# Kernel tuning notes

Hardware: AMD Instinct MI355X
Metric: run time of the kernel (lower is better)

Reference implementation:

```python
import jax, jax.numpy as jnp
import numpy as np

NUM_HEADS = 16


def setup_inputs() -> dict:
    key = jax.random.key(0)
    ks = jax.random.split(key, 8)
    B, S, D = 2, 2048, 1024
    q = jax.random.normal(ks[0], (B, S, D), dtype=jnp.float32)
    k = jax.random.normal(ks[1], (B, S, D), dtype=jnp.float32)
    v = jax.random.normal(ks[2], (B, S, D), dtype=jnp.float32)
    mask = jax.random.randint(ks[3], (1, 1, S, S), 0, 2, dtype=jnp.int32)
    sc = 1.0 / np.sqrt(D)
    wq = jax.random.normal(ks[4], (D, D), dtype=jnp.float32) * sc
    wk = jax.random.normal(ks[5], (D, D), dtype=jnp.float32) * sc
    wv = jax.random.normal(ks[6], (D, D), dtype=jnp.float32) * sc
    wout = jax.random.normal(ks[7], (D, D), dtype=jnp.float32) * sc
    return {"q": q, "k": k, "v": v, "mask": mask,
            "wq": wq, "wk": wk, "wv": wv, "wout": wout}


def reference(q, k, v, mask, wq, wk, wv, wout):
    B, S, D = q.shape
    H = NUM_HEADS
    hd = D // H

    def proj(x, w):
        # nn.Linear(bias=False): x @ w.T, then split heads -> [B,H,S,hd]
        return (x @ w.T).reshape(B, -1, H, hd).transpose(0, 2, 1, 3)

    qh, kh, vh = proj(q, wq), proj(k, wk), proj(v, wv)
    scale = jnp.asarray(hd, q.dtype) ** 0.5
    scores = jnp.einsum('bhqd,bhkd->bhqk', qh, kh) / scale  # [B,H,S,S]
    att = jax.nn.softmax(scores, axis=-1)
    # NOTE: original applies masked_fill AFTER softmax with value -1e-9
    att = jnp.where(mask == 0, jnp.asarray(-1e-9, att.dtype), att)
    out = jnp.einsum('bhqk,bhkd->bhqd', att, vh)  # [B,H,S,hd]
    out = out.transpose(0, 2, 1, 3).reshape(B, S, D)
    return out @ wout.T
```

## Files before the change

### kernel.cpp

```cpp
#include <hip/hip_runtime.h>
#include <stdint.h>


#define BATCH  2
#define S_LEN  2048
#define DMODEL 1024
#define NH     16
#define HD     64

typedef __bf16 bf16_t;
typedef short  short8 __attribute__((ext_vector_type(8)));
typedef float  f32x4  __attribute__((ext_vector_type(4)));

#define AS1 __attribute__((address_space(1)))
#define AS3 __attribute__((address_space(3)))

static constexpr size_t MB = (size_t)1 << 20;
static constexpr size_t WS_REQUIRED = 112 * MB;
#define OFF_XHI(z)  ((size_t)(z) * 16 * MB)
#define OFF_XLO(z)  (OFF_XHI(z) + 8 * MB)
#define OFF_WHI(z)  (48 * MB + (size_t)(z) * 4 * MB)
#define OFF_WLO(z)  (OFF_WHI(z) + 2 * MB)
#define OFF_PHI(z)  (64 * MB + (size_t)(z) * 16 * MB)
#define OFF_PLO(z)  (OFF_PHI(z) + 8 * MB)
#define OFF_OHI     ((size_t)0)
#define OFF_OLO     (8 * MB)
#define OFF_MASKB   (16 * MB)

__device__ __forceinline__ f32x4 mfma_bf16(short8 a, short8 b, f32x4 c) {
    return __builtin_amdgcn_mfma_f32_16x16x32_bf16(a, b, c, 0, 0, 0);
}

__device__ __forceinline__ short8 ld8(const bf16_t* p) {
    return *reinterpret_cast<const short8*>(p);
}

__global__ void cvt_split_kernel(const float* __restrict__ x,
                                 bf16_t* __restrict__ hi, bf16_t* __restrict__ lo,
                                 int n) {
    int i = (blockIdx.x * blockDim.x + threadIdx.x) * 4;
    if (i >= n) return;
    const float4 v = *reinterpret_cast<const float4*>(x + i);
    float s[4] = {v.x, v.y, v.z, v.w};
    ushort hbits[4], lbits[4];
#pragma unroll
    for (int j = 0; j < 4; j++) {
        bf16_t hh = (bf16_t)s[j];
        bf16_t ll = (bf16_t)(s[j] - (float)hh);
        hbits[j] = __builtin_bit_cast(ushort, hh);
        lbits[j] = __builtin_bit_cast(ushort, ll);
    }
    *reinterpret_cast<ushort4*>(hi + i) = ushort4{hbits[0], hbits[1], hbits[2], hbits[3]};
    *reinterpret_cast<ushort4*>(lo + i) = ushort4{lbits[0], lbits[1], lbits[2], lbits[3]};
}

__global__ void cvt_mask_kernel(const int* __restrict__ m, bf16_t* __restrict__ mb, int n) {
    int i = (blockIdx.x * blockDim.x + threadIdx.x) * 4;
    if (i >= n) return;
    const int4 v = *reinterpret_cast<const int4*>(m + i);
    int s[4] = {v.x, v.y, v.z, v.w};
    ushort b[4];
#pragma unroll
    for (int j = 0; j < 4; j++) {
        bf16_t t = (bf16_t)(s[j] ? 1.0f : 0.0f);
        b[j] = __builtin_bit_cast(ushort, t);
    }
    *reinterpret_cast<ushort4*>(mb + i) = ushort4{b[0], b[1], b[2], b[3]};
}

template <int FINAL>
__global__ __launch_bounds__(256, 2) void gemm_split_kernel(char* __restrict__ ws,
                                                            float* __restrict__ fout) {
    __shared__ __align__(16) bf16_t AsH[128 * 32];
    __shared__ __align__(16) bf16_t AsL[128 * 32];
    __shared__ __align__(16) bf16_t BsH[128 * 32];
    __shared__ __align__(16) bf16_t BsL[128 * 32];

    const int z = FINAL ? 3 : blockIdx.z;
    const bf16_t* Ahi = FINAL ? (const bf16_t*)(ws + OFF_OHI) : (const bf16_t*)(ws + OFF_XHI(z));
    const bf16_t* Alo = FINAL ? (const bf16_t*)(ws + OFF_OLO) : (const bf16_t*)(ws + OFF_XLO(z));
    const bf16_t* Bhi = (const bf16_t*)(ws + OFF_WHI(z));
    const bf16_t* Blo = (const bf16_t*)(ws + OFF_WLO(z));
    bf16_t* Ohi = FINAL ? nullptr : (bf16_t*)(ws + OFF_PHI(z));
    bf16_t* Olo = FINAL ? nullptr : (bf16_t*)(ws + OFF_PLO(z));
    const float scale = (!FINAL && z == 0) ? 0.125f : 1.0f;

    const int tid = threadIdx.x;
    const int lane = tid & 63, w = tid >> 6;
    const int wr = w >> 1, wc = w & 1;
    const int fr = lane & 15, fg = lane >> 4;
    const int m0 = blockIdx.x * 128, n0 = blockIdx.y * 128;
    const int K = 1024;

    f32x4 acc[4][4];
#pragma unroll
    for (int i = 0; i < 4; i++)
#pragma unroll
        for (int j = 0; j < 4; j++) acc[i][j] = f32x4{0.f, 0.f, 0.f, 0.f};

    AS3 bf16_t* asAH = (AS3 bf16_t*)AsH;
    AS3 bf16_t* asAL = (AS3 bf16_t*)AsL;
    AS3 bf16_t* asBH = (AS3 bf16_t*)BsH;
    AS3 bf16_t* asBL = (AS3 bf16_t*)BsL;

#pragma unroll 1
    for (int ks = 0; ks < K; ks += 32) {
        __syncthreads();
#pragma unroll
        for (int i = 0; i < 2; i++) {
            const int c = i * 256 + tid;
            const int row = c >> 2;
            const int ce = (c & 3) * 8;
            const size_t gA = (size_t)(m0 + row) * K + ks + ce;
            const size_t gB = (size_t)(n0 + row) * K + ks + ce;
            const size_t d = (size_t)(i * 256 + w * 64) * 8;
            __builtin_amdgcn_global_load_lds((const AS1 void*)(Ahi + gA), (AS3 void*)(asAH + d), 16, 0, 0);
            __builtin_amdgcn_global_load_lds((const AS1 void*)(Alo + gA), (AS3 void*)(asAL + d), 16, 0, 0);
            __builtin_amdgcn_global_load_lds((const AS1 void*)(Bhi + gB), (AS3 void*)(asBH + d), 16, 0, 0);
            __builtin_amdgcn_global_load_lds((const AS1 void*)(Blo + gB), (AS3 void*)(asBL + d), 16, 0, 0);
        }
        __syncthreads();

        short8 afh[4], afl[4], bfh[4], bfl[4];
#pragma unroll
        for (int i = 0; i < 4; i++) {
            const int ao = (wr * 64 + i * 16 + fr) * 32 + fg * 8;
            const int bo = (wc * 64 + i * 16 + fr) * 32 + fg * 8;
            afh[i] = ld8(&AsH[ao]);
            afl[i] = ld8(&AsL[ao]);
            bfh[i] = ld8(&BsH[bo]);
            bfl[i] = ld8(&BsL[bo]);
        }
#pragma unroll
        for (int i = 0; i < 4; i++)
#pragma unroll
            for (int j = 0; j < 4; j++) {
                acc[i][j] = mfma_bf16(afh[i], bfh[j], acc[i][j]);
                acc[i][j] = mfma_bf16(afh[i], bfl[j], acc[i][j]);
                acc[i][j] = mfma_bf16(afl[i], bfh[j], acc[i][j]);
            }
    }

#pragma unroll
    for (int i = 0; i < 4; i++) {
#pragma unroll
        for (int j = 0; j < 4; j++) {
            const int ncol = n0 + wc * 64 + j * 16 + fr;
#pragma unroll
            for (int r = 0; r < 4; r++) {
                const int m = m0 + wr * 64 + i * 16 + fg * 4 + r;
                const float val = acc[i][j][r] * scale;
                if (FINAL) {
                    fout[(size_t)m * DMODEL + ncol] = val;
                } else {
                    const bf16_t h = (bf16_t)val;
                    const bf16_t l = (bf16_t)(val - (float)h);
                    const int b = m >> 11, s = m & (S_LEN - 1);
                    const int hh = ncol >> 6, d = ncol & (HD - 1);
                    size_t idx;
                    if (z == 2) idx = ((size_t)(b * NH + hh) * HD + d) * S_LEN + s;
                    else        idx = ((size_t)(b * NH + hh) * S_LEN + s) * HD + d;
                    Ohi[idx] = h;
                    Olo[idx] = l;
                }
            }
        }
    }
}

__global__ __launch_bounds__(256, 2) void attn_kernel(char* __restrict__ ws) {
    __shared__ __align__(16) bf16_t KsH[2][8 * 64 * 8];
    __shared__ __align__(16) bf16_t KsL[2][8 * 64 * 8];
    __shared__ __align__(16) bf16_t VsH[2][8 * 64 * 8];
    __shared__ __align__(16) bf16_t VsL[2][8 * 64 * 8];

    const bf16_t* Qhi = (const bf16_t*)(ws + OFF_PHI(0));
    const bf16_t* Qlo = (const bf16_t*)(ws + OFF_PLO(0));
    const bf16_t* Khi = (const bf16_t*)(ws + OFF_PHI(1));
    const bf16_t* Klo = (const bf16_t*)(ws + OFF_PLO(1));
    const bf16_t* Vhi = (const bf16_t*)(ws + OFF_PHI(2));
    const bf16_t* Vlo = (const bf16_t*)(ws + OFF_PLO(2));
    const bf16_t* Mb  = (const bf16_t*)(ws + OFF_MASKB);
    bf16_t* Ohi = (bf16_t*)(ws + OFF_OHI);
    bf16_t* Olo = (bf16_t*)(ws + OFF_OLO);

    const int tid = threadIdx.x, lane = tid & 63, w = tid >> 6;
    const int fr = lane & 15, fg = lane >> 4;
    const int bh = blockIdx.y;
    const int q0 = blockIdx.x * 64;
    const int qrow = q0 + w * 16 + fr;
    const size_t qkBase = (size_t)bh * S_LEN * HD;
    const size_t vtBase = (size_t)bh * HD * S_LEN;

    size_t kSrc[2], vSrc[2];
#pragma unroll
    for (int i = 0; i < 2; i++) {
        const int s = i * 256 + tid;
        const int l = s & 63, f = (s >> 6) & 7;
        const int sfr = l & 15, sfg = l >> 4;
        const int cf = f >> 1, kc = f & 1;
        const int r = (cf & 1) * 4 + (sfr & 3) + (sfr >> 2) * 8 + (cf >> 1) * 32;
        kSrc[i] = qkBase + (size_t)r * HD + kc * 32 + sfg * 8;
        vSrc[i] = vtBase + (size_t)((f >> 1) * 16 + sfr) * S_LEN + (f & 1) * 32 + sfg * 8;
    }

    short8 qh[2], ql[2];
#pragma unroll
    for (int kc = 0; kc < 2; kc++) {
        const size_t off = qkBase + (size_t)qrow * HD + kc * 32 + fg * 8;
        qh[kc] = ld8(Qhi + off);
        ql[kc] = ld8(Qlo + off);
    }

    f32x4 acco[4];
#pragma unroll
    for (int df = 0; df < 4; df++) acco[df] = f32x4{0.f, 0.f, 0.f, 0.f};
    float mrun = -__builtin_inff(), lrun = 0.f;

    const size_t mrowBase = (size_t)qrow * S_LEN;

#define STAGE(K0, BUF)                                                                             \
    {                                                                                              \
        _Pragma("unroll") for (int i = 0; i < 2; i++) {                                            \
            const size_t ko = kSrc[i] + (size_t)(K0) * HD;                                         \
            const size_t vo = vSrc[i] + (K0);                                                      \
            const size_t dst = (size_t)(i * 256 + w * 64) * 8;                                     \
            __builtin_amdgcn_global_load_lds((const AS1 void*)(Khi + ko),                          \
                                             (AS3 void*)((AS3 bf16_t*)KsH[BUF] + dst), 16, 0, 0);  \
            __builtin_amdgcn_global_load_lds((const AS1 void*)(Klo + ko),                          \
                                             (AS3 void*)((AS3 bf16_t*)KsL[BUF] + dst), 16, 0, 0);  \
            __builtin_amdgcn_global_load_lds((const AS1 void*)(Vhi + vo),                          \
                                             (AS3 void*)((AS3 bf16_t*)VsH[BUF] + dst), 16, 0, 0);  \
            __builtin_amdgcn_global_load_lds((const AS1 void*)(Vlo + vo),                          \
                                             (AS3 void*)((AS3 bf16_t*)VsL[BUF] + dst), 16, 0, 0);  \
        }                                                                                          \
    }

    STAGE(0, 0)
    short8 mv0Cur = ld8(Mb + mrowBase + fg * 8);
    short8 mv1Cur = ld8(Mb + mrowBase + 32 + fg * 8);
    short8 mv0Nxt = mv0Cur, mv1Nxt = mv1Cur;
    __syncthreads();

    int cur = 0;
#pragma unroll 1
    for (int k0 = 0; k0 < S_LEN; k0 += 64) {
        if (k0 + 64 < S_LEN) {
            STAGE(k0 + 64, cur ^ 1)
            mv0Nxt = ld8(Mb + mrowBase + (k0 + 64) + fg * 8);
            mv1Nxt = ld8(Mb + mrowBase + (k0 + 64) + 32 + fg * 8);
        }

        f32x4 sacc[4];
#pragma unroll
        for (int cf = 0; cf < 4; cf++) sacc[cf] = f32x4{0.f, 0.f, 0.f, 0.f};
        __builtin_amdgcn_s_setprio(1);
#pragma unroll
        for (int cf = 0; cf < 4; cf++) {
#pragma unroll
            for (int kc = 0; kc < 2; kc++) {
                const int fi = cf * 2 + kc;
                const short8 kh = ld8(&KsH[cur][(fi * 64 + lane) * 8]);
                const short8 kl = ld8(&KsL[cur][(fi * 64 + lane) * 8]);
                sacc[cf] = mfma_bf16(kh, qh[kc], sacc[cf]);
                sacc[cf] = mfma_bf16(kl, qh[kc], sacc[cf]);
                sacc[cf] = mfma_bf16(kh, ql[kc], sacc[cf]);
            }
        }
        __builtin_amdgcn_s_setprio(0);

        float mx = sacc[0][0];
#pragma unroll
        for (int cf = 0; cf < 4; cf++)
#pragma unroll
            for (int r = 0; r < 4; r++) mx = fmaxf(mx, sacc[cf][r]);
        mx = fmaxf(mx, __shfl_xor(mx, 16, 64));
        mx = fmaxf(mx, __shfl_xor(mx, 32, 64));
        const float mnew = fmaxf(mrun, mx);
        const float alpha = __expf(mrun - mnew);
        mrun = mnew;

        float p[4][4], psum = 0.f;
#pragma unroll
        for (int cf = 0; cf < 4; cf++)
#pragma unroll
            for (int r = 0; r < 4; r++) {
                p[cf][r] = __expf(sacc[cf][r] - mnew);
                psum += p[cf][r];
            }
        psum += __shfl_xor(psum, 16, 64);
        psum += __shfl_xor(psum, 32, 64);
        lrun = lrun * alpha + psum;
#pragma unroll
        for (int df = 0; df < 4; df++) acco[df] *= alpha;

        short8 phi[2], plo[2];
#pragma unroll
        for (int kc2 = 0; kc2 < 2; kc2++) {
#pragma unroll
            for (int j = 0; j < 8; j++) {
                const int cf = kc2 * 2 + (j >> 2), r = j & 3;
                const float mvf = (float)__builtin_bit_cast(
                    bf16_t, (ushort)((cf >> 1) ? mv1Cur[(cf & 1) * 4 + r] : mv0Cur[(cf & 1) * 4 + r]));
                const float pm = p[cf][r] * mvf;
                const bf16_t h = (bf16_t)pm;
                const bf16_t l = (bf16_t)(pm - (float)h);
                phi[kc2][j] = __builtin_bit_cast(short, h);
                plo[kc2][j] = __builtin_bit_cast(short, l);
            }
        }

        __builtin_amdgcn_s_setprio(1);
#pragma unroll
        for (int kc2 = 0; kc2 < 2; kc2++) {
#pragma unroll
            for (int df = 0; df < 4; df++) {
                const int fi = df * 2 + kc2;
                const short8 vh = ld8(&VsH[cur][(fi * 64 + lane) * 8]);
                const short8 vl = ld8(&VsL[cur][(fi * 64 + lane) * 8]);
                acco[df] = mfma_bf16(vh, phi[kc2], acco[df]);
                acco[df] = mfma_bf16(vl, phi[kc2], acco[df]);
                acco[df] = mfma_bf16(vh, plo[kc2], acco[df]);
            }
        }
        __builtin_amdgcn_s_setprio(0);

        __syncthreads();
        mv0Cur = mv0Nxt;
        mv1Cur = mv1Nxt;
        cur ^= 1;
    }
#undef STAGE

    const int b = bh >> 4, hh = bh & (NH - 1);
    const float inv = 1.0f / lrun;
    const size_t obase = ((size_t)b * S_LEN + qrow) * DMODEL + hh * HD;
#pragma unroll
    for (int df = 0; df < 4; df++) {
#pragma unroll
        for (int r = 0; r < 4; r++) {
            const int d = df * 16 + fg * 4 + r;
            const float o = acco[df][r] * inv;
            const bf16_t h = (bf16_t)o;
            Ohi[obase + d] = h;
            Olo[obase + d] = (bf16_t)(o - (float)h);
        }
    }
}

extern "C" void kernel_launch(void* const* d_in, const int* in_sizes, int n_in,
                              void* d_out, int out_size, void* d_ws, size_t ws_size,
                              hipStream_t stream) {
    (void)in_sizes; (void)n_in; (void)out_size;
    if (ws_size < WS_REQUIRED) return;

    const float* q    = (const float*)d_in[0];
    const float* k    = (const float*)d_in[1];
    const float* v    = (const float*)d_in[2];
    const int*   mask = (const int*)  d_in[3];
    const float* wq   = (const float*)d_in[4];
    const float* wk   = (const float*)d_in[5];
    const float* wv   = (const float*)d_in[6];
    const float* wout = (const float*)d_in[7];
    char* ws = (char*)d_ws;
    float* out = (float*)d_out;

    const size_t nX = (size_t)BATCH * S_LEN * DMODEL;
    const size_t nW = (size_t)DMODEL * DMODEL;
    const size_t nM = (size_t)S_LEN * S_LEN;
    const dim3 blk(256);

    cvt_split_kernel<<<dim3(nX / 1024), blk, 0, stream>>>(q, (bf16_t*)(ws + OFF_XHI(0)), (bf16_t*)(ws + OFF_XLO(0)), (int)nX);
    cvt_split_kernel<<<dim3(nX / 1024), blk, 0, stream>>>(k, (bf16_t*)(ws + OFF_XHI(1)), (bf16_t*)(ws + OFF_XLO(1)), (int)nX);
    cvt_split_kernel<<<dim3(nX / 1024), blk, 0, stream>>>(v, (bf16_t*)(ws + OFF_XHI(2)), (bf16_t*)(ws + OFF_XLO(2)), (int)nX);
    cvt_split_kernel<<<dim3(nW / 1024), blk, 0, stream>>>(wq,   (bf16_t*)(ws + OFF_WHI(0)), (bf16_t*)(ws + OFF_WLO(0)), (int)nW);
    cvt_split_kernel<<<dim3(nW / 1024), blk, 0, stream>>>(wk,   (bf16_t*)(ws + OFF_WHI(1)), (bf16_t*)(ws + OFF_WLO(1)), (int)nW);
    cvt_split_kernel<<<dim3(nW / 1024), blk, 0, stream>>>(wv,   (bf16_t*)(ws + OFF_WHI(2)), (bf16_t*)(ws + OFF_WLO(2)), (int)nW);
    cvt_split_kernel<<<dim3(nW / 1024), blk, 0, stream>>>(wout, (bf16_t*)(ws + OFF_WHI(3)), (bf16_t*)(ws + OFF_WLO(3)), (int)nW);

    gemm_split_kernel<0><<<dim3(32, 8, 3), blk, 0, stream>>>(ws, nullptr);

    cvt_mask_kernel<<<dim3(nM / 1024), blk, 0, stream>>>(mask, (bf16_t*)(ws + OFF_MASKB), (int)nM);

    attn_kernel<<<dim3(S_LEN / 64, BATCH * NH), blk, 0, stream>>>(ws);

    gemm_split_kernel<1><<<dim3(32, 8, 1), blk, 0, stream>>>(ws, out);
}
```

Baseline: 441.7 us.

## Single-buffer V tiles, fold log2e into Q scale, add lazy softmax rescaling

The V shared-memory tiles drop from double to single buffering. V is now loaded at the start of each iteration, and an added barrier before the PV MFMAs waits for it, which lowers LDS use per block. The Q projection scale now includes log2(e), so the softmax uses exp2f. The running max and accumulator rescale are skipped unless some row's max grows by more than 8. The aim is less LDS pressure and fewer exp and multiply operations, at the cost of exposing the V load latency and adding an extra barrier every iteration.

```diff
diff --git a/kernel.cpp b/kernel.cpp
--- a/kernel.cpp
+++ b/kernel.cpp
@@ -83,7 +83,7 @@
     const bf16_t* Blo = (const bf16_t*)(ws + OFF_WLO(z));
     bf16_t* Ohi = FINAL ? nullptr : (bf16_t*)(ws + OFF_PHI(z));
     bf16_t* Olo = FINAL ? nullptr : (bf16_t*)(ws + OFF_PLO(z));
-    const float scale = (!FINAL && z == 0) ? 0.125f : 1.0f;
+    const float scale = (!FINAL && z == 0) ? 0.18033688011112042f : 1.0f;
 
     const int tid = threadIdx.x;
     const int lane = tid & 63, w = tid >> 6;
@@ -171,8 +171,8 @@
 __global__ __launch_bounds__(256, 2) void attn_kernel(char* __restrict__ ws) {
     __shared__ __align__(16) bf16_t KsH[2][8 * 64 * 8];
     __shared__ __align__(16) bf16_t KsL[2][8 * 64 * 8];
-    __shared__ __align__(16) bf16_t VsH[2][8 * 64 * 8];
-    __shared__ __align__(16) bf16_t VsL[2][8 * 64 * 8];
+    __shared__ __align__(16) bf16_t VsH[8 * 64 * 8];
+    __shared__ __align__(16) bf16_t VsL[8 * 64 * 8];
 
     const bf16_t* Qhi = (const bf16_t*)(ws + OFF_PHI(0));
     const bf16_t* Qlo = (const bf16_t*)(ws + OFF_PLO(0));
@@ -219,24 +219,30 @@
 
     const size_t mrowBase = (size_t)qrow * S_LEN;
 
-#define STAGE(K0, BUF)                                                                             \
+#define STAGE_K(K0, BUF)                                                                           \
     {                                                                                              \
         _Pragma("unroll") for (int i = 0; i < 2; i++) {                                            \
             const size_t ko = kSrc[i] + (size_t)(K0) * HD;                                         \
-            const size_t vo = vSrc[i] + (K0);                                                      \
             const size_t dst = (size_t)(i * 256 + w * 64) * 8;                                     \
             __builtin_amdgcn_global_load_lds((const AS1 void*)(Khi + ko),                          \
                                              (AS3 void*)((AS3 bf16_t*)KsH[BUF] + dst), 16, 0, 0);  \
             __builtin_amdgcn_global_load_lds((const AS1 void*)(Klo + ko),                          \
                                              (AS3 void*)((AS3 bf16_t*)KsL[BUF] + dst), 16, 0, 0);  \
+        }                                                                                          \
+    }
+#define STAGE_V(K0)                                                                                \
+    {                                                                                              \
+        _Pragma("unroll") for (int i = 0; i < 2; i++) {                                            \
+            const size_t vo = vSrc[i] + (K0);                                                      \
+            const size_t dst = (size_t)(i * 256 + w * 64) * 8;                                     \
             __builtin_amdgcn_global_load_lds((const AS1 void*)(Vhi + vo),                          \
-                                             (AS3 void*)((AS3 bf16_t*)VsH[BUF] + dst), 16, 0, 0);  \
+                                             (AS3 void*)((AS3 bf16_t*)VsH + dst), 16, 0, 0);       \
             __builtin_amdgcn_global_load_lds((const AS1 void*)(Vlo + vo),                          \
-                                             (AS3 void*)((AS3 bf16_t*)VsL[BUF] + dst), 16, 0, 0);  \
+                                             (AS3 void*)((AS3 bf16_t*)VsL + dst), 16, 0, 0);       \
         }                                                                                          \
     }
 
-    STAGE(0, 0)
+    STAGE_K(0, 0)
     short8 mv0Cur = ld8(Mb + mrowBase + fg * 8);
     short8 mv1Cur = ld8(Mb + mrowBase + 32 + fg * 8);
     short8 mv0Nxt = mv0Cur, mv1Nxt = mv1Cur;
@@ -245,8 +251,9 @@
     int cur = 0;
 #pragma unroll 1
     for (int k0 = 0; k0 < S_LEN; k0 += 64) {
+        STAGE_V(k0)
         if (k0 + 64 < S_LEN) {
-            STAGE(k0 + 64, cur ^ 1)
+            STAGE_K(k0 + 64, cur ^ 1)
             mv0Nxt = ld8(Mb + mrowBase + (k0 + 64) + fg * 8);
             mv1Nxt = ld8(Mb + mrowBase + (k0 + 64) + 32 + fg * 8);
         }
@@ -276,23 +283,26 @@
             for (int r = 0; r < 4; r++) mx = fmaxf(mx, sacc[cf][r]);
         mx = fmaxf(mx, __shfl_xor(mx, 16, 64));
         mx = fmaxf(mx, __shfl_xor(mx, 32, 64));
-        const float mnew = fmaxf(mrun, mx);
-        const float alpha = __expf(mrun - mnew);
-        mrun = mnew;
+        if (!__all(mx <= mrun + 8.0f)) {
+            const float mnew = fmaxf(mrun, mx);
+            const float alpha = exp2f(mrun - mnew);
+            mrun = mnew;
+            lrun *= alpha;
+#pragma unroll
+            for (int df = 0; df < 4; df++) acco[df] *= alpha;
+        }
 
         float p[4][4], psum = 0.f;
 #pragma unroll
         for (int cf = 0; cf < 4; cf++)
 #pragma unroll
             for (int r = 0; r < 4; r++) {
-                p[cf][r] = __expf(sacc[cf][r] - mnew);
+                p[cf][r] = exp2f(sacc[cf][r] - mrun);
                 psum += p[cf][r];
             }
         psum += __shfl_xor(psum, 16, 64);
         psum += __shfl_xor(psum, 32, 64);
-        lrun = lrun * alpha + psum;
-#pragma unroll
-        for (int df = 0; df < 4; df++) acco[df] *= alpha;
+        lrun += psum;
 
         short8 phi[2], plo[2];
 #pragma unroll
@@ -310,14 +320,16 @@
             }
         }
 
+        __syncthreads();
+
         __builtin_amdgcn_s_setprio(1);
 #pragma unroll
         for (int kc2 = 0; kc2 < 2; kc2++) {
 #pragma unroll
             for (int df = 0; df < 4; df++) {
                 const int fi = df * 2 + kc2;
-                const short8 vh = ld8(&VsH[cur][(fi * 64 + lane) * 8]);
-                const short8 vl = ld8(&VsL[cur][(fi * 64 + lane) * 8]);
+                const short8 vh = ld8(&VsH[(fi * 64 + lane) * 8]);
+                const short8 vl = ld8(&VsL[(fi * 64 + lane) * 8]);
                 acco[df] = mfma_bf16(vh, phi[kc2], acco[df]);
                 acco[df] = mfma_bf16(vl, phi[kc2], acco[df]);
                 acco[df] = mfma_bf16(vh, plo[kc2], acco[df]);
@@ -330,7 +342,8 @@
         mv1Cur = mv1Nxt;
         cur ^= 1;
     }
-#undef STAGE
+#undef STAGE_K
+#undef STAGE_V
 
     const int b = bh >> 4, hh = bh & (NH - 1);
     const float inv = 1.0f / lrun;
```

New measurement: 438.1 us. No clear change (-0.8%).
